# Optimization experiments

Hardware: AMD Instinct MI355X
Metric: run time of the kernel (lower is better)

## Reference

```python
import jax, jax.numpy as jnp
import numpy as np

LAGRANGE_ORDER = 5  # fixed, as in the torch module


def _lagrange_weights(alpha):
    """Vectorised Lagrange weights of length L+1. alpha: [B,N] -> [B,N,L+1]."""
    L = LAGRANGE_ORDER
    j = jnp.arange(L + 1, dtype=alpha.dtype)
    u = alpha[..., None] - j                          # [B,N,L+1]
    denom = j[:, None] - j[None, :]                   # [L+1,L+1]
    mask = ~jnp.eye(L + 1, dtype=bool)
    num = jnp.where(mask, u[..., None, :], jnp.ones_like(u)[..., None, :])
    den = jnp.where(mask, denom, jnp.ones_like(denom))
    return (num / den).prod(axis=-1)                  # [B,N,L+1]


def setup_inputs() -> dict:
    key = jax.random.key(0)
    k1, k2, k3 = jax.random.split(key, 3)
    B, N = 16, 16384
    # fractional period in samples, in [40, 100) -> max floor(f0)=99, K=99+5+3=107<=108
    f0 = 40.0 + 60.0 * jax.random.uniform(k1, (B, N), dtype=jnp.float32)
    x = jax.random.normal(k2, (B, N), dtype=jnp.float32)
    l_b = jax.random.uniform(k3, (B, N, 2), dtype=jnp.float32)  # (g, p) in [0,1]
    return {"f0": f0, "x": x, "l_b": l_b, "K": 108}


def reference(f0, x, l_b, K):
    B, N = x.shape
    L = LAGRANGE_ORDER
    # design_loop: (g, p) -> loop taps [b0, a1]; gain capped <1 for stability
    g = 0.99 * l_b[..., 0]
    p = l_b[..., 1]
    b0 = g * (1.0 - p)                                # [B,N]
    a1 = g * p
    # tune_f0: subtract low-frequency phase delay of (b0 + a1 z^-1)
    f0c = f0 - a1 / (b0 + a1 + 1e-7)
    # Lagrange centre & weights
    z = jnp.floor(f0c).astype(jnp.int32)
    z_center = z - L // 2                             # [B,N]
    alpha = f0c - z_center.astype(f0.dtype)
    w = _lagrange_weights(alpha)                      # [B,N,L+1]
    # compute_resonator_matrix: loop filter convolved with fractional delay -> block [B,N,L+2]
    block = (b0[..., None] * jnp.pad(w, ((0, 0), (0, 0), (0, 1)))
             + a1[..., None] * jnp.pad(w, ((0, 0), (0, 0), (1, 0))))
    # scatter (-block) into A; LPC lag k+1 lives in column k
    cols = z_center[..., None] - 1 + jnp.arange(L + 2)  # [B,N,L+2]
    cols = jnp.clip(cols, 0, K - 1)
    A = jnp.zeros((B, N, K), x.dtype).at[
        jnp.arange(B)[:, None, None], jnp.arange(N)[None, :, None], cols
    ].add(-block)
    # sample_wise_lpc: y[n] = x[n] - sum_k A[n,k] * y[n-1-k], zero init state
    def step(buf, inp):
        a_n, x_n = inp                                 # [B,K], [B]
        y_n = x_n - jnp.sum(a_n * buf, axis=-1)
        buf = jnp.concatenate([y_n[:, None], buf[:, :-1]], axis=1)
        return buf, y_n
    buf0 = jnp.zeros((B, K), x.dtype)
    _, ys = jax.lax.scan(step, buf0, (A.transpose(1, 0, 2), x.T))  # ys: [N,B]
    return ys.T
```

## Files before the change

### kernel.cpp

```cpp
#include <hip/hip_runtime.h>
#include <math.h>


#define B_    16
#define N_    16384
#define S_    16
#define NSEG  1024
#define NITER 28
#define RUNS  104
#define CHUNK 37
#define HROWS 263

#define TG_FLOATS (B_ * S_ * RUNS * RUNS)
#define ST_FLOATS (B_ * S_ * RUNS)
#define CG_FLOATS (B_ * S_ * NSEG * 8)

__device__ __forceinline__ void diffks_coeffs(float f0v, float lbg, float lbp,
                                              int n, float4& lo, float4& hi) {
  float g  = 0.99f * lbg;
  float p  = lbp;
  float b0 = g * (1.0f - p);
  float a1 = g * p;
  float f0c = f0v - a1 / (b0 + a1 + 1e-7f);
  int   zc  = (int)floorf(f0c) - 2;
  float alpha = f0c - (float)zc;
  float u0 = alpha;
  float u1 = alpha - 1.0f;
  float u2 = alpha - 2.0f;
  float u3 = alpha - 3.0f;
  float u4 = alpha - 4.0f;
  float u5 = alpha - 5.0f;
  float w0 = u1 * u2 * u3 * u4 * u5 * (-1.0f / 120.0f);
  float w1 = u0 * u2 * u3 * u4 * u5 * ( 1.0f /  24.0f);
  float w2 = u0 * u1 * u3 * u4 * u5 * (-1.0f /  12.0f);
  float w3 = u0 * u1 * u2 * u4 * u5 * ( 1.0f /  12.0f);
  float w4 = u0 * u1 * u2 * u3 * u5 * (-1.0f /  24.0f);
  float w5 = u0 * u1 * u2 * u3 * u4 * ( 1.0f / 120.0f);
  lo.x = b0 * w0;
  lo.y = fmaf(b0, w1, a1 * w0);
  lo.z = fmaf(b0, w2, a1 * w1);
  lo.w = fmaf(b0, w3, a1 * w2);
  hi.x = fmaf(b0, w4, a1 * w3);
  hi.y = fmaf(b0, w5, a1 * w4);
  hi.z = a1 * w5;
  hi.w = __int_as_float((n - 6 - zc) & 255);
}

__global__ __launch_bounds__(1024) void diffks_phase1(
    const float* __restrict__ f0, const float* __restrict__ lb,
    const float* __restrict__ x, float* __restrict__ Tg,
    float* __restrict__ Cg) {
  const int bs = blockIdx.x;
  const int b  = bs >> 4, s = bs & 15;
  const int n0 = s << 10;
  const int tid = threadIdx.x;

  __shared__ __align__(16) float hist[HROWS * RUNS];
  __shared__ float4 sLo[NSEG], sHi[NSEG];
  __shared__ float  sX[NSEG];

  {
    const size_t gi = (size_t)b * N_ + n0 + tid;
    const float2 lv = ((const float2*)lb)[gi];
    float4 lo, hi;
    diffks_coeffs(f0[gi], lv.x, lv.y, tid, lo, hi);
    sLo[tid] = lo; sHi[tid] = hi; sX[tid] = x[gi];
    float4* __restrict__ C = (float4*)Cg + (size_t)bs * 2 * NSEG;
    C[2 * tid]     = lo;
    C[2 * tid + 1] = hi;
  }
  for (int i = tid; i < (HROWS * RUNS) / 4; i += 1024)
    ((float4*)hist)[i] = float4{0.0f, 0.0f, 0.0f, 0.0f};
  __syncthreads();
  if (tid < 103) hist[(255 - tid) * RUNS + tid] = 1.0f;
  __syncthreads();

  {
    const int w    = tid >> 6;
    const int lane = tid & 63;
    const int cl   = 2 * lane;
    const bool act = (lane < 52);
    const bool px  = (lane == 51);
    float* __restrict__ hcol = hist + cl;

    for (int t = 0; t < 32; ++t) {
#pragma unroll
      for (int u = 0; u < 2; ++u) {
        const int p = 32 * t + 2 * w + u;
        const float4 lo = sLo[p];
        const float4 hi = sHi[p];
        const float  xv = sX[p];
        if (act) {
          const int base = __float_as_int(hi.w);
          const float* __restrict__ hr = hcol + base * RUNS;
          float2 acc;
          acc.x = 0.0f;
          acc.y = px ? xv : 0.0f;
          const float c[7] = {hi.z, hi.y, hi.x, lo.w, lo.z, lo.y, lo.x};
#pragma unroll
          for (int m = 0; m < 7; ++m) {
            const float2 v = *(const float2*)(hr + m * RUNS);
            acc.x = fmaf(c[m], v.x, acc.x);
            acc.y = fmaf(c[m], v.y, acc.y);
          }
          const int wsl = p & 255;
          *(float2*)(hcol + wsl * RUNS) = acc;
          if (wsl < 7)
            *(float2*)(hcol + (wsl + 256) * RUNS) = acc;
        }
      }
      __syncthreads();
    }
  }

  float* __restrict__ T = Tg + (size_t)bs * RUNS * RUNS;
  for (int idx = tid; idx < RUNS * RUNS; idx += 1024) {
    const int r = idx / RUNS;
    const int j = idx - r * RUNS;
    T[idx] = (j < 103) ? hist[((255 - j) & 255) * RUNS + r] : 0.0f;
  }
}

#define P2_STEP(s_, tv_)                                                      \
  {                                                                           \
    if (q == 0) states[((size_t)b * S_ + (s_)) * RUNS + j] = cur[j];          \
    float acc = 0.0f;                                                         \
    _Pragma("unroll")                                                         \
    for (int k = 0; k < 13; ++k) acc = fmaf(tv_[k], cur[r0 + k], acc);        \
    if ((s_) + 2 < S_) {                                                      \
      const float* __restrict__ Tn = Tb + (size_t)((s_) + 2) * RUNS * RUNS;   \
      _Pragma("unroll")                                                       \
      for (int k = 0; k < 13; ++k) tv_[k] = Tn[(size_t)(r0 + k) * RUNS + j];  \
    }                                                                         \
    part[q][j] = acc;                                                         \
    __syncthreads();                                                          \
    if (q == 0) {                                                             \
      float v = 0.0f;                                                         \
      _Pragma("unroll")                                                       \
      for (int qq = 0; qq < 8; ++qq) v += part[qq][j];                        \
      cur[j] = (j < 103) ? v : 1.0f;                                          \
    }                                                                         \
    __syncthreads();                                                          \
  }

__global__ __launch_bounds__(832) void diffks_phase2(
    const float* __restrict__ Tg, float* __restrict__ states) {
  const int b   = blockIdx.x;
  const int tid = threadIdx.x;
  const int j   = tid % RUNS;
  const int q   = tid / RUNS;
  const int r0  = 13 * q;
  __shared__ float cur[RUNS];
  __shared__ float part[8][105];
  if (tid < 103) cur[tid] = 0.0f;
  if (tid == 103) cur[103] = 1.0f;
  __syncthreads();

  const float* __restrict__ Tb = Tg + (size_t)b * S_ * RUNS * RUNS;
  float tvA[13], tvB[13];
#pragma unroll
  for (int k = 0; k < 13; ++k)
    tvA[k] = Tb[(size_t)(r0 + k) * RUNS + j];
#pragma unroll
  for (int k = 0; k < 13; ++k)
    tvB[k] = Tb[(size_t)RUNS * RUNS + (size_t)(r0 + k) * RUNS + j];

#pragma unroll
  for (int sp = 0; sp < 8; ++sp) {
    P2_STEP(2 * sp,     tvA)
    P2_STEP(2 * sp + 1, tvB)
  }
}

__global__ __launch_bounds__(256) void diffks_phase3(
    const float* __restrict__ Cg, const float* __restrict__ x,
    const float* __restrict__ states, float* __restrict__ y) {
  const int bs = blockIdx.x;
  const int b  = bs >> 4, s = bs & 15;
  const int n0 = s << 10;
  const int tid = threadIdx.x;

  __shared__ __align__(16) float ring[512];
  __shared__ float4 sC[2 * NSEG];
  __shared__ float  sX[NSEG];
  __shared__ float  sY[NSEG];

#pragma unroll
  for (int k = 0; k < 2; ++k) ring[tid + 256 * k] = 0.0f;
  {
    const size_t gb = (size_t)b * N_ + n0;
    const float*  __restrict__ xb = x + gb;
    const float4* __restrict__ cb = (const float4*)Cg + (size_t)bs * 2 * NSEG;
    float4 v0[4], v1[4]; float vx[4];
#pragma unroll
    for (int k = 0; k < 4; ++k) {
      const int i = tid + 256 * k;
      v0[k] = cb[2 * i]; v1[k] = cb[2 * i + 1]; vx[k] = xb[i];
    }
#pragma unroll
    for (int k = 0; k < 4; ++k) {
      const int i = tid + 256 * k;
      sC[2 * i] = v0[k]; sC[2 * i + 1] = v1[k]; sX[i] = vx[k];
    }
  }
  __syncthreads();
  const float* __restrict__ st = states + (size_t)bs * RUNS;
  if (tid < 103) {
    const float v = st[tid];
    ring[255 - tid] = v;
    ring[511 - tid] = v;
  }
  __syncthreads();

  if (tid < 64) {
    const int lane = tid;
    const bool act = (lane < CHUNK);
    for (int t = 0; t < NITER; ++t) {
      const int p = t * CHUNK + lane;
      if (act && p < NSEG) {
        const float4 lo = sC[2 * p];
        const float4 hi = sC[2 * p + 1];
        const float  xv = sX[p];
        const int base = __float_as_int(hi.w);
        const float r0 = ring[base + 0];
        const float r1 = ring[base + 1];
        const float r2 = ring[base + 2];
        const float r3 = ring[base + 3];
        const float r4 = ring[base + 4];
        const float r5 = ring[base + 5];
        const float r6 = ring[base + 6];
        const float s0 = fmaf(lo.x, r6, xv);
        const float s1 = fmaf(lo.y, r5, lo.z * r4);
        const float s2 = fmaf(lo.w, r3, hi.x * r2);
        const float s3 = fmaf(hi.y, r1, hi.z * r0);
        const float yv = (s0 + s1) + (s2 + s3);
        const int wsl = p & 255;
        ring[wsl]       = yv;
        ring[wsl + 256] = yv;
        sY[p] = yv;
      }
      __builtin_amdgcn_wave_barrier();
      asm volatile("" ::: "memory");
    }
  }
  __syncthreads();

  float4* __restrict__ yb = (float4*)(y + (size_t)b * N_ + n0);
  yb[tid] = ((const float4*)sY)[tid];
}

__global__ __launch_bounds__(256) void diffks_coeff_fb(
    const float* __restrict__ f0, const float* __restrict__ lb,
    float* __restrict__ cw, int total, int Nmask) {
  int idx = blockIdx.x * blockDim.x + threadIdx.x;
  if (idx >= total) return;
  float4 lo, hi;
  diffks_coeffs(f0[idx], lb[2 * idx], lb[2 * idx + 1], idx & Nmask, lo, hi);
  float4* out4 = (float4*)cw;
  out4[2 * idx]     = lo;
  out4[2 * idx + 1] = hi;
}

__global__ __launch_bounds__(64) void diffks_scan_fb(
    const float* __restrict__ x, const float* __restrict__ cw,
    float* __restrict__ y, int N) {
  const int b    = blockIdx.x;
  const int lane = threadIdx.x;
  __shared__ float ring[512];
#pragma unroll
  for (int i = 0; i < 8; ++i) ring[lane + 64 * i] = 0.0f;
  __builtin_amdgcn_wave_barrier();
  asm volatile("" ::: "memory");
  const float4* __restrict__ c4 = (const float4*)(cw + (size_t)b * N * 8);
  const float*  __restrict__ xb = x + (size_t)b * N;
  float*        __restrict__ yb = y + (size_t)b * N;
  const bool act = (lane < CHUNK);
  const int nIter = (N + CHUNK - 1) / CHUNK;
  for (int t = 0; t < nIter; ++t) {
    const int n = t * CHUNK + lane;
    if (act && n < N) {
      const float4 lo = c4[2 * n];
      const float4 hi = c4[2 * n + 1];
      const float  xv = xb[n];
      const int base = __float_as_int(hi.w);
      const float r0 = ring[base + 0];
      const float r1 = ring[base + 1];
      const float r2 = ring[base + 2];
      const float r3 = ring[base + 3];
      const float r4 = ring[base + 4];
      const float r5 = ring[base + 5];
      const float r6 = ring[base + 6];
      const float s0 = fmaf(lo.x, r6, xv);
      const float s1 = fmaf(lo.y, r5, lo.z * r4);
      const float s2 = fmaf(lo.w, r3, hi.x * r2);
      const float s3 = fmaf(hi.y, r1, hi.z * r0);
      const float yv = (s0 + s1) + (s2 + s3);
      ring[n & 255]         = yv;
      ring[(n & 255) + 256] = yv;
      yb[n] = yv;
    }
    __builtin_amdgcn_wave_barrier();
    asm volatile("" ::: "memory");
  }
}

extern "C" void kernel_launch(void* const* d_in, const int* in_sizes, int n_in,
                              void* d_out, int out_size, void* d_ws, size_t ws_size,
                              hipStream_t stream) {
  const float* f0 = (const float*)d_in[0];
  const float* x  = (const float*)d_in[1];
  const float* lb = (const float*)d_in[2];
  float* out = (float*)d_out;

  const int total = in_sizes[0];
  const size_t need = (size_t)(TG_FLOATS + ST_FLOATS + CG_FLOATS) * 4;

  if (total == B_ * N_ && ws_size >= need) {
    float* Tg = (float*)d_ws;
    float* st = Tg + TG_FLOATS;
    float* Cg = st + ST_FLOATS;
    diffks_phase1<<<B_ * S_, 1024, 0, stream>>>(f0, lb, x, Tg, Cg);
    diffks_phase2<<<B_, 832, 0, stream>>>(Tg, st);
    diffks_phase3<<<B_ * S_, 256, 0, stream>>>(Cg, x, st, out);
  } else {
    const int N = total / B_;
    float* cw = (float*)d_ws;
    diffks_coeff_fb<<<(total + 255) / 256, 256, 0, stream>>>(f0, lb, cw, total, N - 1);
    diffks_scan_fb<<<B_, 64, 0, stream>>>(x, cw, out, N);
  }
}
```

Baseline: 110.5 us.

## Merge three scan phases into one cooperative kernel with grid syncs

Replaces the three-kernel pipeline (segment transfer matrices, cross-segment state propagation, final per-segment scan) with a single cooperative launch that uses grid-wide syncs between the phases. Coefficients and the input segment stay in shared memory across phases, so the Cg round trip through global memory and two kernel launches go away. Phase 3 now recomputes the segment scan from shared coefficients with a single wave instead of reading stored data. The cost is grid sync overhead, and most blocks sit idle during the serial state propagation done by the s==15 blocks. If the cooperative launch fails, the code falls back to the old three kernels.

Measured after the change: 333.5 us. 202% more time.

```diff
diff --git a/kernel.cpp b/kernel.cpp
--- a/kernel.cpp
+++ b/kernel.cpp
@@ -1,5 +1,8 @@
 #include <hip/hip_runtime.h>
+#include <hip/hip_cooperative_groups.h>
 #include <math.h>
+
+namespace cg = cooperative_groups;
 
 
 #define B_    16
@@ -44,6 +47,187 @@
   hi.y = fmaf(b0, w5, a1 * w4);
   hi.z = a1 * w5;
   hi.w = __int_as_float((n - 6 - zc) & 255);
+}
+
+#define P2M_STEP(s_, tv_)                                                     \
+  {                                                                           \
+    if (p2a) {                                                                \
+      if (q == 0) states[((size_t)b * S_ + (s_)) * RUNS + j] = cur[j];        \
+      float acc = 0.0f;                                                       \
+      _Pragma("unroll")                                                       \
+      for (int k = 0; k < 13; ++k) acc = fmaf(tv_[k], cur[r0 + k], acc);      \
+      if ((s_) + 2 < S_) {                                                    \
+        const float* __restrict__ Tn = Tb + (size_t)((s_) + 2) * RUNS * RUNS; \
+        _Pragma("unroll")                                                     \
+        for (int k = 0; k < 13; ++k) tv_[k] = Tn[(size_t)(r0 + k) * RUNS + j];\
+      }                                                                       \
+      part[q][j] = acc;                                                       \
+    }                                                                         \
+    __syncthreads();                                                          \
+    if (p2a && q == 0) {                                                      \
+      float v = 0.0f;                                                         \
+      _Pragma("unroll")                                                       \
+      for (int qq = 0; qq < 8; ++qq) v += part[qq][j];                        \
+      cur[j] = (j < 103) ? v : 1.0f;                                          \
+    }                                                                         \
+    __syncthreads();                                                          \
+  }
+
+__global__ __launch_bounds__(1024) void diffks_merged(
+    const float* __restrict__ f0, const float* __restrict__ lb,
+    const float* __restrict__ x, float* __restrict__ Tg,
+    float* __restrict__ states, float* __restrict__ y) {
+  const int bs = blockIdx.x;
+  const int b  = bs >> 4, s = bs & 15;
+  const int n0 = s << 10;
+  const int tid = threadIdx.x;
+
+  __shared__ __align__(16) float hist[HROWS * RUNS];
+  __shared__ __align__(16) float4 sLo[NSEG], sHi[NSEG];
+  __shared__ float  sX[NSEG];
+
+  {
+    const size_t gi = (size_t)b * N_ + n0 + tid;
+    const float2 lv = ((const float2*)lb)[gi];
+    float4 lo, hi;
+    diffks_coeffs(f0[gi], lv.x, lv.y, tid, lo, hi);
+    sLo[tid] = lo; sHi[tid] = hi; sX[tid] = x[gi];
+  }
+  for (int i = tid; i < (HROWS * RUNS) / 4; i += 1024)
+    ((float4*)hist)[i] = float4{0.0f, 0.0f, 0.0f, 0.0f};
+  __syncthreads();
+  if (tid < 103) hist[(255 - tid) * RUNS + tid] = 1.0f;
+  __syncthreads();
+
+  {
+    const int w    = tid >> 6;
+    const int lane = tid & 63;
+    const int cl   = 2 * lane;
+    const bool act = (lane < 52);
+    const bool px  = (lane == 51);
+    float* __restrict__ hcol = hist + cl;
+
+    for (int t = 0; t < 32; ++t) {
+#pragma unroll
+      for (int u = 0; u < 2; ++u) {
+        const int p = 32 * t + 2 * w + u;
+        const float4 lo = sLo[p];
+        const float4 hi = sHi[p];
+        const float  xv = sX[p];
+        if (act) {
+          const int base = __float_as_int(hi.w);
+          const float* __restrict__ hr = hcol + base * RUNS;
+          float2 acc;
+          acc.x = 0.0f;
+          acc.y = px ? xv : 0.0f;
+          const float c[7] = {hi.z, hi.y, hi.x, lo.w, lo.z, lo.y, lo.x};
+#pragma unroll
+          for (int m = 0; m < 7; ++m) {
+            const float2 v = *(const float2*)(hr + m * RUNS);
+            acc.x = fmaf(c[m], v.x, acc.x);
+            acc.y = fmaf(c[m], v.y, acc.y);
+          }
+          const int wsl = p & 255;
+          *(float2*)(hcol + wsl * RUNS) = acc;
+          if (wsl < 7)
+            *(float2*)(hcol + (wsl + 256) * RUNS) = acc;
+        }
+      }
+      __syncthreads();
+    }
+  }
+
+  {
+    float* __restrict__ T = Tg + (size_t)bs * RUNS * RUNS;
+    for (int idx = tid; idx < RUNS * RUNS; idx += 1024) {
+      const int r = idx / RUNS;
+      const int j = idx - r * RUNS;
+      T[idx] = (j < 103) ? hist[((255 - j) & 255) * RUNS + r] : 0.0f;
+    }
+  }
+  __syncthreads();
+  if (tid < 512) hist[tid] = 0.0f;
+  __threadfence();
+  cg::this_grid().sync();
+
+  if (s == 15) {
+    const int j   = tid % RUNS;
+    const int q   = tid / RUNS;
+    const int r0  = 13 * q;
+    const bool p2a = (tid < 832);
+    float* __restrict__ cur = hist + 2048;
+    float (*__restrict__ part)[105] = (float (*)[105])(hist + 2176);
+
+    if (tid < 103) cur[tid] = 0.0f;
+    if (tid == 103) cur[103] = 1.0f;
+    __syncthreads();
+
+    const float* __restrict__ Tb = Tg + (size_t)b * S_ * RUNS * RUNS;
+    float tvA[13], tvB[13];
+    if (p2a) {
+#pragma unroll
+      for (int k = 0; k < 13; ++k)
+        tvA[k] = Tb[(size_t)(r0 + k) * RUNS + j];
+#pragma unroll
+      for (int k = 0; k < 13; ++k)
+        tvB[k] = Tb[(size_t)RUNS * RUNS + (size_t)(r0 + k) * RUNS + j];
+    }
+
+#pragma unroll
+    for (int sp = 0; sp < 8; ++sp) {
+      P2M_STEP(2 * sp,     tvA)
+      P2M_STEP(2 * sp + 1, tvB)
+    }
+  }
+  __threadfence();
+  cg::this_grid().sync();
+
+  if (s != 0 && tid < 103) {
+    const float v = states[(size_t)bs * RUNS + tid];
+    hist[255 - tid] = v;
+    hist[511 - tid] = v;
+  }
+  __syncthreads();
+
+  if (tid < 64) {
+    const int lane = tid;
+    const bool act = (lane < CHUNK);
+    float* __restrict__ ring = hist;
+    float* __restrict__ sY   = hist + 512;
+    for (int t = 0; t < NITER; ++t) {
+      const int p = t * CHUNK + lane;
+      if (act && p < NSEG) {
+        const float4 lo = sLo[p];
+        const float4 hi = sHi[p];
+        const float  xv = sX[p];
+        const int base = __float_as_int(hi.w);
+        const float r0 = ring[base + 0];
+        const float r1 = ring[base + 1];
+        const float r2 = ring[base + 2];
+        const float r3 = ring[base + 3];
+        const float r4 = ring[base + 4];
+        const float r5 = ring[base + 5];
+        const float r6 = ring[base + 6];
+        const float s0 = fmaf(lo.x, r6, xv);
+        const float s1 = fmaf(lo.y, r5, lo.z * r4);
+        const float s2 = fmaf(lo.w, r3, hi.x * r2);
+        const float s3 = fmaf(hi.y, r1, hi.z * r0);
+        const float yv = (s0 + s1) + (s2 + s3);
+        const int wsl = p & 255;
+        ring[wsl]       = yv;
+        ring[wsl + 256] = yv;
+        sY[p] = yv;
+      }
+      __builtin_amdgcn_wave_barrier();
+      asm volatile("" ::: "memory");
+    }
+  }
+  __syncthreads();
+
+  if (tid < 256) {
+    float4* __restrict__ yb = (float4*)(y + (size_t)b * N_ + n0);
+    yb[tid] = ((const float4*)(hist + 512))[tid];
+  }
 }
 
 __global__ __launch_bounds__(1024) void diffks_phase1(
@@ -319,6 +503,15 @@
     float* Tg = (float*)d_ws;
     float* st = Tg + TG_FLOATS;
     float* Cg = st + ST_FLOATS;
+
+    void* args[] = {(void*)&f0, (void*)&lb, (void*)&x,
+                    (void*)&Tg, (void*)&st, (void*)&out};
+    hipError_t e = hipLaunchCooperativeKernel((const void*)diffks_merged,
+                                              dim3(B_ * S_), dim3(1024),
+                                              args, 0, stream);
+    if (e == hipSuccess) return;
+    (void)hipGetLastError();
+
     diffks_phase1<<<B_ * S_, 1024, 0, stream>>>(f0, lb, x, Tg, Cg);
     diffks_phase2<<<B_, 832, 0, stream>>>(Tg, st);
     diffks_phase3<<<B_ * S_, 256, 0, stream>>>(Cg, x, st, out);
```
